# Kernel tuning notes

Measured on AMD Instinct MI355X. Metric: run time of the kernel, lower is better.

## Reference

```python
import jax, jax.numpy as jnp
import numpy as np

N = 50000        # nodes
E = 800000       # edges (avg degree 16)
H = 128          # hidden_nf
IN_NODE = 11     # in_node_nf
IN_EDGE = 4      # in_edge_nf
L = 4            # n_layers


def _lin_init(key, fan_in, fan_out, layers=None):
    shape = (fan_in, fan_out) if layers is None else (layers, fan_in, fan_out)
    return jax.random.normal(key, shape, dtype=jnp.float32) / np.sqrt(fan_in)


def setup_inputs() -> dict:
    key = jax.random.key(0)
    ks = jax.random.split(key, 16)
    edge_in = 2 * H + 1 + IN_EDGE   # [h_row, h_col, radial, edge_attr]
    node_in = H + H + IN_NODE       # [h, agg, h0]
    return {
        "h0": jax.random.normal(ks[0], (N, IN_NODE), dtype=jnp.float32),
        "x": jax.random.normal(ks[1], (N, 3), dtype=jnp.float32),
        "edge_index": jax.random.randint(ks[2], (2, E), 0, N),
        "edge_attr": jax.random.normal(ks[3], (E, IN_EDGE), dtype=jnp.float32),
        "node_mask": jnp.ones((N, 1), dtype=jnp.float32),
        "edge_mask": jnp.ones((E, 1), dtype=jnp.float32),
        "n_nodes": N,
        "emb_w": _lin_init(ks[4], IN_NODE, H),
        "emb_b": jnp.zeros((H,), dtype=jnp.float32),
        "ew1": _lin_init(ks[5], edge_in, H, L),
        "eb1": jnp.zeros((L, H), dtype=jnp.float32),
        "ew2": _lin_init(ks[6], H, H, L),
        "eb2": jnp.zeros((L, H), dtype=jnp.float32),
        "nw1": _lin_init(ks[7], node_in, H, L),
        "nb1": jnp.zeros((L, H), dtype=jnp.float32),
        "nw2": _lin_init(ks[8], H, H, L),
        "nb2": jnp.zeros((L, H), dtype=jnp.float32),
    }


def reference(h0, x, edge_index, edge_attr, node_mask, edge_mask, n_nodes,
              emb_w, emb_b, ew1, eb1, ew2, eb2, nw1, nb1, nw2, nb2):
    row, col = edge_index[0], edge_index[1]
    num_nodes = h0.shape[0]
    # coord2radial (coords never updated since coord_model is not called)
    coord_diff = x[row] - x[col]                               # [E, 3]
    radial = jnp.sum(coord_diff * coord_diff, axis=1, keepdims=True)  # [E, 1]

    h = h0 @ emb_w + emb_b                                     # embedding, [N, H]
    for i in range(L):
        # edge model
        edge_in = jnp.concatenate([h[row], h[col], radial, edge_attr], axis=1)
        m = jax.nn.silu(edge_in @ ew1[i] + eb1[i])
        m = jax.nn.silu(m @ ew2[i] + eb2[i])
        m = m * edge_mask                                      # [E, H]
        # node model: scatter-sum messages, concat with h and node_attr=h0
        agg = jax.ops.segment_sum(m, row, num_segments=num_nodes)  # [N, H]
        node_in = jnp.concatenate([h, agg, h0], axis=1)
        out = jax.nn.silu(node_in @ nw1[i] + nb1[i]) @ nw2[i] + nb2[i]
        h = h + out                                            # recurrent residual
    return h
```

## Files before the change

### kernel.cpp

```cpp
#include <hip/hip_runtime.h>

#define NN 50000
#define NE 800000
#define HD 128
#define INN 11
#define NL 4
#define NG16 3125
#define BTS 132
#define K1S 292

typedef __attribute__((ext_vector_type(8))) short bf16x8;
typedef __attribute__((ext_vector_type(4))) float f32x4;

__device__ __forceinline__ float silu_f(float x) {
    return x * __builtin_amdgcn_rcpf(1.0f + __expf(-x));
}

__device__ __forceinline__ short f2bf(float x) {
    unsigned u = __float_as_uint(x);
    return (short)((u + 0x7FFFu + ((u >> 16) & 1u)) >> 16);
}
__device__ __forceinline__ unsigned f2bf2u(float lo, float hi) {
    unsigned a = __float_as_uint(lo), b = __float_as_uint(hi);
    a = (a + 0x7FFFu + ((a >> 16) & 1u)) >> 16;
    b = (b + 0x7FFFu + ((b >> 16) & 1u)) & 0xFFFF0000u;
    return a | b;
}
__device__ __forceinline__ bf16x8 pack8(float4 a, float4 b) {
    bf16x8 r;
    r[0] = f2bf(a.x); r[1] = f2bf(a.y); r[2] = f2bf(a.z); r[3] = f2bf(a.w);
    r[4] = f2bf(b.x); r[5] = f2bf(b.y); r[6] = f2bf(b.z); r[7] = f2bf(b.w);
    return r;
}

__global__ __launch_bounds__(256) void embed_kernel(
    const float* __restrict__ h0, const float* __restrict__ w,
    const float* __restrict__ b, float* __restrict__ h)
{
    int idx = blockIdx.x * 256 + threadIdx.x;
    if (idx >= NN * HD) return;
    int n = idx >> 7, j = idx & 127;
    float acc = b[j];
    #pragma unroll
    for (int k = 0; k < INN; ++k)
        acc += h0[n * INN + k] * w[k * HD + j];
    h[idx] = acc;
}

__global__ __launch_bounds__(256) void csr_zero(int* __restrict__ cnt)
{
    int i = blockIdx.x * 256 + threadIdx.x;
    if (i < NN) cnt[i] = 0;
}

__global__ __launch_bounds__(256) void csr_hist(const int* __restrict__ ei, int* __restrict__ cnt)
{
    int e = blockIdx.x * 256 + threadIdx.x;
    atomicAdd(&cnt[ei[e]], 1);
}

__global__ __launch_bounds__(1024) void csr_scan(
    const int* __restrict__ cnt, int* __restrict__ rowptr, int* __restrict__ cursor)
{
    __shared__ int part[1024];
    int t = threadIdx.x;
    int base = t * 49;
    int s = 0;
    for (int i = 0; i < 49; ++i) { int j = base + i; if (j < NN) s += cnt[j]; }
    part[t] = s;
    __syncthreads();
    for (int off = 1; off < 1024; off <<= 1) {
        int v = (t >= off) ? part[t - off] : 0;
        __syncthreads();
        part[t] += v;
        __syncthreads();
    }
    int run = (t == 0) ? 0 : part[t - 1];
    for (int i = 0; i < 49; ++i) {
        int j = base + i;
        if (j < NN) { rowptr[j] = run; cursor[j] = run; run += cnt[j]; }
    }
    if (t == 1023) rowptr[NN] = part[1023];
}

__global__ __launch_bounds__(256) void csr_fill(
    const int* __restrict__ ei, int* __restrict__ cursor, int* __restrict__ eidx)
{
    int e = blockIdx.x * 256 + threadIdx.x;
    int r = ei[e];
    int p = atomicAdd(&cursor[r], 1);
    eidx[p] = e;
}

__global__ __launch_bounds__(256) void edge_pre(
    const int* __restrict__ ei, const int* __restrict__ eidx,
    const float* __restrict__ x, const float* __restrict__ emask,
    int4* __restrict__ ed_p)
{
    int p = blockIdx.x * 256 + threadIdx.x;
    int e = eidx[p];
    int r = ei[e], c = ei[NE + e];
    float dx = x[3 * r]     - x[3 * c];
    float dy = x[3 * r + 1] - x[3 * c + 1];
    float dz = x[3 * r + 2] - x[3 * c + 2];
    float rad = dx * dx + dy * dy + dz * dz;
    ed_p[p] = make_int4(r * 64, c * 64, __float_as_int(rad), __float_as_int(emask[e]));
}

__global__ __launch_bounds__(1024) void vpad_zero(unsigned* __restrict__ vb32)
{
    vb32[(size_t)NE * 64 + threadIdx.x] = 0u;
}

__global__ __launch_bounds__(512) void tu_mfma(
    const float* __restrict__ h, const float* __restrict__ ew1_l,
    short* __restrict__ tb, short* __restrict__ ub)
{
    __shared__ __align__(16) short BT[128 * BTS];
    const float* wsrc = ew1_l + (blockIdx.y ? 128 * HD : 0);
    short* outp = blockIdx.y ? ub : tb;
    for (int i = threadIdx.x; i < 128 * 128; i += 512) {
        int c = i >> 7, k = i & 127;
        BT[c * BTS + k] = f2bf(wsrc[k * HD + c]);
    }
    int wv = threadIdx.x >> 6, lane = threadIdx.x & 63;
    int ln15 = lane & 15, quad = lane >> 4;
    __syncthreads();

    for (int g = blockIdx.x * 8 + wv; g < NG16; g += gridDim.x * 8) {
        int row = g * 16 + ln15;
        const float* hrow = h + row * HD;
        bf16x8 afr[4];
        #pragma unroll
        for (int kt = 0; kt < 4; ++kt) {
            float4 x0 = *(const float4*)(hrow + kt * 32 + quad * 8);
            float4 x1 = *(const float4*)(hrow + kt * 32 + quad * 8 + 4);
            afr[kt] = pack8(x0, x1);
        }
        #pragma unroll
        for (int ct = 0; ct < 8; ++ct) {
            f32x4 acc = {0.f, 0.f, 0.f, 0.f};
            #pragma unroll
            for (int kt = 0; kt < 4; ++kt) {
                bf16x8 bfr = *(const bf16x8*)&BT[(ct * 16 + ln15) * BTS + kt * 32 + quad * 8];
                acc = __builtin_amdgcn_mfma_f32_16x16x32_bf16(afr[kt], bfr, acc, 0, 0, 0);
            }
            int col = ct * 16 + ln15;
            #pragma unroll
            for (int r4 = 0; r4 < 4; ++r4) {
                int orow = g * 16 + quad * 4 + r4;
                outp[orow * HD + col] = f2bf(acc[r4]);
            }
        }
    }
}

__global__ __launch_bounds__(512) void edge_v_kernel(
    const short* __restrict__ tb, const short* __restrict__ ub,
    const int4* __restrict__ ed_p, const int* __restrict__ eidx,
    const float* __restrict__ eattr,
    const float* __restrict__ ew1_l, const float* __restrict__ eb1_l,
    short* __restrict__ vbuf)
{
    int cp = threadIdx.x & 63;
    int c0 = cp * 2;
    float wr0  = ew1_l[256 * HD + c0],     wr1  = ew1_l[256 * HD + c0 + 1];
    float wa00 = ew1_l[257 * HD + c0],     wa01 = ew1_l[257 * HD + c0 + 1];
    float wa10 = ew1_l[258 * HD + c0],     wa11 = ew1_l[258 * HD + c0 + 1];
    float wa20 = ew1_l[259 * HD + c0],     wa21 = ew1_l[259 * HD + c0 + 1];
    float wa30 = ew1_l[260 * HD + c0],     wa31 = ew1_l[260 * HD + c0 + 1];
    float b10  = eb1_l[c0],                b11  = eb1_l[c0 + 1];

    const unsigned* tb32 = (const unsigned*)tb;
    const unsigned* ub32 = (const unsigned*)ub;
    const float4*   ea4  = (const float4*)eattr;
    unsigned*       vb32 = (unsigned*)vbuf;

    int w  = (blockIdx.x * 512 + threadIdx.x) >> 6;
    int nw = gridDim.x * 8;

    for (int p0 = w * 4; p0 < NE; p0 += nw * 4) {
        int4 edv[4]; unsigned twv[4], uwv[4]; float4 eav[4];
        #pragma unroll
        for (int j = 0; j < 4; ++j) edv[j] = ed_p[p0 + j];
        #pragma unroll
        for (int j = 0; j < 4; ++j) {
            twv[j] = tb32[edv[j].x + cp];
            uwv[j] = ub32[edv[j].y + cp];
            eav[j] = ea4[eidx[p0 + j]];
        }
        #pragma unroll
        for (int j = 0; j < 4; ++j) {
            float rad = __int_as_float(edv[j].z);
            float t0 = __uint_as_float(twv[j] << 16);
            float t1 = __uint_as_float(twv[j] & 0xFFFF0000u);
            float u0 = __uint_as_float(uwv[j] << 16);
            float u1 = __uint_as_float(uwv[j] & 0xFFFF0000u);
            float s0 = t0 + u0 + rad * wr0 + eav[j].x * wa00 + eav[j].y * wa10
                     + eav[j].z * wa20 + eav[j].w * wa30 + b10;
            float s1 = t1 + u1 + rad * wr1 + eav[j].x * wa01 + eav[j].y * wa11
                     + eav[j].z * wa21 + eav[j].w * wa31 + b11;
            vb32[(size_t)(p0 + j) * 64 + cp] = f2bf2u(silu_f(s0), silu_f(s1));
        }
    }
}

__global__ __launch_bounds__(512) void edge_agg_kernel(
    const short* __restrict__ vbuf, const int4* __restrict__ ed_p,
    const int* __restrict__ rowptr,
    const float* __restrict__ ew2_l, const float* __restrict__ eb2_l,
    short* __restrict__ aggb)
{
    __shared__ __align__(16) short BT[128 * BTS];
    __shared__ float s_b2[128];

    for (int i = threadIdx.x; i < 128 * 128; i += 512) {
        int k = i >> 7, n = i & 127;
        BT[n * BTS + k] = f2bf(ew2_l[i]);
    }
    if (threadIdx.x < 128) s_b2[threadIdx.x] = eb2_l[threadIdx.x];

    int lane = threadIdx.x & 63;
    int wv   = threadIdx.x >> 6;
    int ln15 = lane & 15;
    int quad = lane >> 4;
    __syncthreads();

    for (int n = blockIdx.x * 8 + wv; n < NN; n += gridDim.x * 8) {
        int s = rowptr[n], en = rowptr[n + 1];

        float sums[8];
        #pragma unroll
        for (int ct = 0; ct < 8; ++ct) sums[ct] = 0.f;

        for (int base = s; base < en; base += 16) {
            const short* vrow = vbuf + (size_t)(base + ln15) * HD + quad * 8;
            bf16x8 afr[4];
            #pragma unroll
            for (int kt = 0; kt < 4; ++kt)
                afr[kt] = *(const bf16x8*)(vrow + kt * 32);

            int pr = base + quad * 4;
            float mk0 = (pr + 0 < en) ? __int_as_float(ed_p[pr + 0].w) : 0.f;
            float mk1 = (pr + 1 < en) ? __int_as_float(ed_p[pr + 1].w) : 0.f;
            float mk2 = (pr + 2 < en) ? __int_as_float(ed_p[pr + 2].w) : 0.f;
            float mk3 = (pr + 3 < en) ? __int_as_float(ed_p[pr + 3].w) : 0.f;

            #pragma unroll
            for (int ct = 0; ct < 8; ++ct) {
                f32x4 acc = {0.f, 0.f, 0.f, 0.f};
                #pragma unroll
                for (int kt = 0; kt < 4; ++kt) {
                    bf16x8 bfr = *(const bf16x8*)&BT[(ct * 16 + ln15) * BTS + kt * 32 + quad * 8];
                    acc = __builtin_amdgcn_mfma_f32_16x16x32_bf16(afr[kt], bfr, acc, 0, 0, 0);
                }
                float b2c = s_b2[ct * 16 + ln15];
                sums[ct] += silu_f(acc[0] + b2c) * mk0 + silu_f(acc[1] + b2c) * mk1
                          + silu_f(acc[2] + b2c) * mk2 + silu_f(acc[3] + b2c) * mk3;
            }
        }

        #pragma unroll
        for (int ct = 0; ct < 8; ++ct) {
            float v = sums[ct];
            v += __shfl_xor(v, 16, 64);
            v += __shfl_xor(v, 32, 64);
            sums[ct] = v;
        }
        float vA = (quad & 2) ? ((quad & 1) ? sums[6] : sums[4])
                              : ((quad & 1) ? sums[2] : sums[0]);
        float vB = (quad & 2) ? ((quad & 1) ? sums[7] : sums[5])
                              : ((quad & 1) ? sums[3] : sums[1]);
        int colA = quad * 32 + ln15;
        aggb[(size_t)n * HD + colA]      = f2bf(vA);
        aggb[(size_t)n * HD + colA + 16] = f2bf(vB);
    }
}

__global__ __launch_bounds__(512) void nk1_mfma(
    const float* __restrict__ h, const short* __restrict__ aggb,
    const float* __restrict__ h0,
    const float* __restrict__ nw1_l, const float* __restrict__ nb1_l,
    short* __restrict__ qb)
{
    __shared__ __align__(16) short BT[64 * K1S];
    int c0 = blockIdx.y * 64;
    for (int i = threadIdx.x; i < 64 * 288; i += 512) {
        int c = i / 288, k = i - c * 288;
        BT[c * K1S + k] = (k < 267) ? f2bf(nw1_l[k * HD + c0 + c]) : (short)0;
    }
    int wv = threadIdx.x >> 6, lane = threadIdx.x & 63;
    int ln15 = lane & 15, quad = lane >> 4;
    __syncthreads();

    for (int g = blockIdx.x * 8 + wv; g < NG16; g += gridDim.x * 8) {
        int row = g * 16 + ln15;
        const float* hrow = h + row * HD;
        bf16x8 afr[9];
        #pragma unroll
        for (int kt = 0; kt < 4; ++kt) {
            float4 x0 = *(const float4*)(hrow + kt * 32 + quad * 8);
            float4 x1 = *(const float4*)(hrow + kt * 32 + quad * 8 + 4);
            afr[kt] = pack8(x0, x1);
        }
        #pragma unroll
        for (int kt = 0; kt < 4; ++kt)
            afr[4 + kt] = *(const bf16x8*)(aggb + (size_t)row * HD + kt * 32 + quad * 8);
        {
            bf16x8 a8 = {0, 0, 0, 0, 0, 0, 0, 0};
            if (quad == 0) {
                #pragma unroll
                for (int jj = 0; jj < 8; ++jj) a8[jj] = f2bf(h0[row * INN + jj]);
            } else if (quad == 1) {
                #pragma unroll
                for (int jj = 0; jj < 3; ++jj) a8[jj] = f2bf(h0[row * INN + 8 + jj]);
            }
            afr[8] = a8;
        }
        #pragma unroll
        for (int ct = 0; ct < 4; ++ct) {
            f32x4 acc = {0.f, 0.f, 0.f, 0.f};
            #pragma unroll
            for (int kt = 0; kt < 9; ++kt) {
                bf16x8 bfr = *(const bf16x8*)&BT[(ct * 16 + ln15) * K1S + kt * 32 + quad * 8];
                acc = __builtin_amdgcn_mfma_f32_16x16x32_bf16(afr[kt], bfr, acc, 0, 0, 0);
            }
            int col = c0 + ct * 16 + ln15;
            float b = nb1_l[col];
            #pragma unroll
            for (int r4 = 0; r4 < 4; ++r4) {
                int orow = g * 16 + quad * 4 + r4;
                qb[orow * HD + col] = f2bf(silu_f(acc[r4] + b));
            }
        }
    }
}

__global__ __launch_bounds__(512) void nk2_mfma(
    const short* __restrict__ qb, const float* __restrict__ nw2_l,
    const float* __restrict__ nb2_l, float* __restrict__ h)
{
    __shared__ __align__(16) short BT[128 * BTS];
    for (int i = threadIdx.x; i < 128 * 128; i += 512) {
        int c = i >> 7, k = i & 127;
        BT[c * BTS + k] = f2bf(nw2_l[k * HD + c]);
    }
    int wv = threadIdx.x >> 6, lane = threadIdx.x & 63;
    int ln15 = lane & 15, quad = lane >> 4;
    __syncthreads();

    for (int g = blockIdx.x * 8 + wv; g < NG16; g += gridDim.x * 8) {
        int row = g * 16 + ln15;
        bf16x8 afr[4];
        #pragma unroll
        for (int kt = 0; kt < 4; ++kt)
            afr[kt] = *(const bf16x8*)(qb + row * HD + kt * 32 + quad * 8);

        #pragma unroll
        for (int ct = 0; ct < 8; ++ct) {
            f32x4 acc = {0.f, 0.f, 0.f, 0.f};
            #pragma unroll
            for (int kt = 0; kt < 4; ++kt) {
                bf16x8 bfr = *(const bf16x8*)&BT[(ct * 16 + ln15) * BTS + kt * 32 + quad * 8];
                acc = __builtin_amdgcn_mfma_f32_16x16x32_bf16(afr[kt], bfr, acc, 0, 0, 0);
            }
            int col = ct * 16 + ln15;
            float b = nb2_l[col];
            #pragma unroll
            for (int r4 = 0; r4 < 4; ++r4) {
                int orow = g * 16 + quad * 4 + r4;
                h[orow * HD + col] += acc[r4] + b;
            }
        }
    }
}

extern "C" void kernel_launch(void* const* d_in, const int* in_sizes, int n_in,
                              void* d_out, int out_size, void* d_ws, size_t ws_size,
                              hipStream_t stream)
{
    const float* h0    = (const float*)d_in[0];
    const float* x     = (const float*)d_in[1];
    const int*   ei    = (const int*)d_in[2];
    const float* eattr = (const float*)d_in[3];
    const float* emask = (const float*)d_in[5];
    const float* emb_w = (const float*)d_in[7];
    const float* emb_b = (const float*)d_in[8];
    const float* ew1   = (const float*)d_in[9];
    const float* eb1   = (const float*)d_in[10];
    const float* ew2   = (const float*)d_in[11];
    const float* eb2   = (const float*)d_in[12];
    const float* nw1   = (const float*)d_in[13];
    const float* nb1   = (const float*)d_in[14];
    const float* nw2   = (const float*)d_in[15];
    const float* nb2   = (const float*)d_in[16];

    float* h = (float*)d_out;

    short*  tb     = (short*)d_ws;
    short*  ub     = tb + (size_t)NN * HD;
    short*  aggb   = ub + (size_t)NN * HD;
    short*  vbuf   = aggb + (size_t)NN * HD;
    int4*   ed_p   = (int4*)(vbuf + (size_t)(NE + 16) * HD);
    int*    rowptr = (int*)(ed_p + NE);
    int*    cnt    = rowptr + NN + 1;
    int*    cursor = cnt + NN;
    int*    eidx   = cursor + NN;
    short*  qb     = tb;

    csr_zero<<<(NN + 255) / 256, 256, 0, stream>>>(cnt);
    csr_hist<<<NE / 256, 256, 0, stream>>>(ei, cnt);
    csr_scan<<<1, 1024, 0, stream>>>(cnt, rowptr, cursor);
    csr_fill<<<NE / 256, 256, 0, stream>>>(ei, cursor, eidx);
    edge_pre<<<NE / 256, 256, 0, stream>>>(ei, eidx, x, emask, ed_p);
    vpad_zero<<<1, 1024, 0, stream>>>((unsigned*)vbuf);

    embed_kernel<<<(NN * HD + 255) / 256, 256, 0, stream>>>(h0, emb_w, emb_b, h);

    dim3 gtu(128, 2);
    dim3 gn1(128, 2);
    for (int l = 0; l < NL; ++l) {
        tu_mfma<<<gtu, 512, 0, stream>>>(h, ew1 + l * 261 * HD, tb, ub);
        edge_v_kernel<<<1024, 512, 0, stream>>>(tb, ub, ed_p, eidx, eattr,
            ew1 + l * 261 * HD, eb1 + l * HD, vbuf);
        edge_agg_kernel<<<1024, 512, 0, stream>>>(vbuf, ed_p, rowptr,
            ew2 + l * HD * HD, eb2 + l * HD, aggb);
        nk1_mfma<<<gn1, 512, 0, stream>>>(h, aggb, h0,
            nw1 + l * 267 * HD, nb1 + l * HD, qb);
        nk2_mfma<<<128, 512, 0, stream>>>(qb, nw2 + l * HD * HD, nb2 + l * HD, h);
    }
}
```

Before: 1.559 ms.

## Parallelize CSR prefix scan, fold edge bias into node projection, pack edge math

Replaces the single-block serial CSR scan with a three-kernel multi-block scan (block sums, scan of partials, per-block emit) so the one-off CSR build no longer runs on a single workgroup. It also adds the first edge-layer bias to the per-node projection output in tu_mfma, taking it out of the per-edge loop. The per-edge linear terms are rewritten with 2-wide float vectors so the compiler can emit packed FMAs. The costs are two extra kernel launches and an extra bf16 rounding of the bias inside the node projection.

```diff
diff --git a/kernel.cpp b/kernel.cpp
--- a/kernel.cpp
+++ b/kernel.cpp
@@ -8,9 +8,11 @@
 #define NG16 3125
 #define BTS 132
 #define K1S 292
+#define NB  196
 
 typedef __attribute__((ext_vector_type(8))) short bf16x8;
 typedef __attribute__((ext_vector_type(4))) float f32x4;
+typedef __attribute__((ext_vector_type(2))) float f32x2;
 
 __device__ __forceinline__ float silu_f(float x) {
     return x * __builtin_amdgcn_rcpf(1.0f + __expf(-x));
@@ -59,28 +61,62 @@
     atomicAdd(&cnt[ei[e]], 1);
 }
 
-__global__ __launch_bounds__(1024) void csr_scan(
-    const int* __restrict__ cnt, int* __restrict__ rowptr, int* __restrict__ cursor)
-{
-    __shared__ int part[1024];
+__global__ __launch_bounds__(256) void csr_blocksum(
+    const int* __restrict__ cnt, int* __restrict__ bsum)
+{
+    __shared__ int red[4];
+    int j = blockIdx.x * 256 + threadIdx.x;
+    int v = (j < NN) ? cnt[j] : 0;
+    #pragma unroll
+    for (int off = 1; off < 64; off <<= 1) v += __shfl_xor(v, off, 64);
+    int lane = threadIdx.x & 63, wv = threadIdx.x >> 6;
+    if (lane == 0) red[wv] = v;
+    __syncthreads();
+    if (threadIdx.x == 0)
+        bsum[blockIdx.x] = red[0] + red[1] + red[2] + red[3];
+}
+
+__global__ __launch_bounds__(256) void csr_scanpart(
+    const int* __restrict__ bsum, int* __restrict__ boff, int* __restrict__ rowptr)
+{
+    __shared__ int part[256];
     int t = threadIdx.x;
-    int base = t * 49;
-    int s = 0;
-    for (int i = 0; i < 49; ++i) { int j = base + i; if (j < NN) s += cnt[j]; }
-    part[t] = s;
-    __syncthreads();
-    for (int off = 1; off < 1024; off <<= 1) {
-        int v = (t >= off) ? part[t - off] : 0;
+    int v = (t < NB) ? bsum[t] : 0;
+    part[t] = v;
+    __syncthreads();
+    #pragma unroll
+    for (int off = 1; off < 256; off <<= 1) {
+        int tmp = (t >= off) ? part[t - off] : 0;
         __syncthreads();
-        part[t] += v;
+        part[t] += tmp;
         __syncthreads();
     }
-    int run = (t == 0) ? 0 : part[t - 1];
-    for (int i = 0; i < 49; ++i) {
-        int j = base + i;
-        if (j < NN) { rowptr[j] = run; cursor[j] = run; run += cnt[j]; }
-    }
-    if (t == 1023) rowptr[NN] = part[1023];
+    if (t < NB) boff[t] = part[t] - v;
+    if (t == NB - 1) rowptr[NN] = part[t];
+}
+
+__global__ __launch_bounds__(256) void csr_emit(
+    const int* __restrict__ cnt, const int* __restrict__ boff,
+    int* __restrict__ rowptr, int* __restrict__ cursor)
+{
+    __shared__ int part[256];
+    int t = threadIdx.x;
+    int j = blockIdx.x * 256 + t;
+    int v = (j < NN) ? cnt[j] : 0;
+    part[t] = v;
+    __syncthreads();
+    #pragma unroll
+    for (int off = 1; off < 256; off <<= 1) {
+        int tmp = (t >= off) ? part[t - off] : 0;
+        __syncthreads();
+        part[t] += tmp;
+        __syncthreads();
+    }
+    if (j < NN) {
+        int r = boff[blockIdx.x] + part[t] - v;
+        rowptr[j] = r;
+        cursor[j] = r;
+    }
 }
 
 __global__ __launch_bounds__(256) void csr_fill(
@@ -114,6 +150,7 @@
 
 __global__ __launch_bounds__(512) void tu_mfma(
     const float* __restrict__ h, const float* __restrict__ ew1_l,
+    const float* __restrict__ eb1_l,
     short* __restrict__ tb, short* __restrict__ ub)
 {
     __shared__ __align__(16) short BT[128 * BTS];
@@ -146,10 +183,11 @@
                 acc = __builtin_amdgcn_mfma_f32_16x16x32_bf16(afr[kt], bfr, acc, 0, 0, 0);
             }
             int col = ct * 16 + ln15;
+            float bb = blockIdx.y ? 0.f : eb1_l[col];
             #pragma unroll
             for (int r4 = 0; r4 < 4; ++r4) {
                 int orow = g * 16 + quad * 4 + r4;
-                outp[orow * HD + col] = f2bf(acc[r4]);
+                outp[orow * HD + col] = f2bf(acc[r4] + bb);
             }
         }
     }
@@ -159,17 +197,16 @@
     const short* __restrict__ tb, const short* __restrict__ ub,
     const int4* __restrict__ ed_p, const int* __restrict__ eidx,
     const float* __restrict__ eattr,
-    const float* __restrict__ ew1_l, const float* __restrict__ eb1_l,
+    const float* __restrict__ ew1_l,
     short* __restrict__ vbuf)
 {
     int cp = threadIdx.x & 63;
     int c0 = cp * 2;
-    float wr0  = ew1_l[256 * HD + c0],     wr1  = ew1_l[256 * HD + c0 + 1];
-    float wa00 = ew1_l[257 * HD + c0],     wa01 = ew1_l[257 * HD + c0 + 1];
-    float wa10 = ew1_l[258 * HD + c0],     wa11 = ew1_l[258 * HD + c0 + 1];
-    float wa20 = ew1_l[259 * HD + c0],     wa21 = ew1_l[259 * HD + c0 + 1];
-    float wa30 = ew1_l[260 * HD + c0],     wa31 = ew1_l[260 * HD + c0 + 1];
-    float b10  = eb1_l[c0],                b11  = eb1_l[c0 + 1];
+    f32x2 wr2  = *(const f32x2*)&ew1_l[256 * HD + c0];
+    f32x2 wa02 = *(const f32x2*)&ew1_l[257 * HD + c0];
+    f32x2 wa12 = *(const f32x2*)&ew1_l[258 * HD + c0];
+    f32x2 wa22 = *(const f32x2*)&ew1_l[259 * HD + c0];
+    f32x2 wa32 = *(const f32x2*)&ew1_l[260 * HD + c0];
 
     const unsigned* tb32 = (const unsigned*)tb;
     const unsigned* ub32 = (const unsigned*)ub;
@@ -192,15 +229,15 @@
         #pragma unroll
         for (int j = 0; j < 4; ++j) {
             float rad = __int_as_float(edv[j].z);
-            float t0 = __uint_as_float(twv[j] << 16);
-            float t1 = __uint_as_float(twv[j] & 0xFFFF0000u);
-            float u0 = __uint_as_float(uwv[j] << 16);
-            float u1 = __uint_as_float(uwv[j] & 0xFFFF0000u);
-            float s0 = t0 + u0 + rad * wr0 + eav[j].x * wa00 + eav[j].y * wa10
-                     + eav[j].z * wa20 + eav[j].w * wa30 + b10;
-            float s1 = t1 + u1 + rad * wr1 + eav[j].x * wa01 + eav[j].y * wa11
-                     + eav[j].z * wa21 + eav[j].w * wa31 + b11;
-            vb32[(size_t)(p0 + j) * 64 + cp] = f2bf2u(silu_f(s0), silu_f(s1));
+            f32x2 s;
+            s.x = __uint_as_float(twv[j] << 16)        + __uint_as_float(uwv[j] << 16);
+            s.y = __uint_as_float(twv[j] & 0xFFFF0000u) + __uint_as_float(uwv[j] & 0xFFFF0000u);
+            s += rad * wr2;
+            s += eav[j].x * wa02;
+            s += eav[j].y * wa12;
+            s += eav[j].z * wa22;
+            s += eav[j].w * wa32;
+            vb32[(size_t)(p0 + j) * 64 + cp] = f2bf2u(silu_f(s.x), silu_f(s.y));
         }
     }
 }
@@ -406,11 +443,15 @@
     int*    cnt    = rowptr + NN + 1;
     int*    cursor = cnt + NN;
     int*    eidx   = cursor + NN;
+    int*    bsum   = eidx + NE;
+    int*    boff   = bsum + NB;
     short*  qb     = tb;
 
     csr_zero<<<(NN + 255) / 256, 256, 0, stream>>>(cnt);
     csr_hist<<<NE / 256, 256, 0, stream>>>(ei, cnt);
-    csr_scan<<<1, 1024, 0, stream>>>(cnt, rowptr, cursor);
+    csr_blocksum<<<NB, 256, 0, stream>>>(cnt, bsum);
+    csr_scanpart<<<1, 256, 0, stream>>>(bsum, boff, rowptr);
+    csr_emit<<<NB, 256, 0, stream>>>(cnt, boff, rowptr, cursor);
     csr_fill<<<NE / 256, 256, 0, stream>>>(ei, cursor, eidx);
     edge_pre<<<NE / 256, 256, 0, stream>>>(ei, eidx, x, emask, ed_p);
     vpad_zero<<<1, 1024, 0, stream>>>((unsigned*)vbuf);
@@ -420,9 +461,9 @@
     dim3 gtu(128, 2);
     dim3 gn1(128, 2);
     for (int l = 0; l < NL; ++l) {
-        tu_mfma<<<gtu, 512, 0, stream>>>(h, ew1 + l * 261 * HD, tb, ub);
+        tu_mfma<<<gtu, 512, 0, stream>>>(h, ew1 + l * 261 * HD, eb1 + l * HD, tb, ub);
         edge_v_kernel<<<1024, 512, 0, stream>>>(tb, ub, ed_p, eidx, eattr,
-            ew1 + l * 261 * HD, eb1 + l * HD, vbuf);
+            ew1 + l * 261 * HD, vbuf);
         edge_agg_kernel<<<1024, 512, 0, stream>>>(vbuf, ed_p, rowptr,
             ew2 + l * HD * HD, eb2 + l * HD, aggb);
         nk1_mfma<<<gn1, 512, 0, stream>>>(h, aggb, h0,
```

After: 1.451 ms. 1.07x faster.
